# Kernel optimization log

Measured on AMD Instinct MI355X. Metric: run time of the kernel, lower is better.

## Reference

```python
import jax, jax.numpy as jnp
import numpy as np

N_BATCHES = 32
N_LABELS = 100


def setup_inputs() -> dict:
    key = jax.random.key(0)
    ks = jax.random.split(key, 7)
    N, D, P = 16384, 2048, 256
    x = jax.random.normal(ks[0], (N, D), dtype=jnp.float32)
    label = jax.random.randint(ks[1], (N,), 0, N_LABELS, dtype=jnp.int64)
    label_batch = jnp.sort(jax.random.randint(ks[2], (N,), 0, N_BATCHES, dtype=jnp.int64))
    W1_w = jax.random.normal(ks[3], (P, D), dtype=jnp.float32) * 0.02
    W1_b = jax.random.normal(ks[4], (P,), dtype=jnp.float32) * 0.02
    W2_w = jax.random.normal(ks[5], (P, D), dtype=jnp.float32) * 0.02
    W2_b = jax.random.normal(ks[6], (P,), dtype=jnp.float32) * 0.02
    return {"x": x, "label": label, "label_batch": label_batch,
            "W1_w": W1_w, "W1_b": W1_b, "W2_w": W2_w, "W2_b": W2_b}


def _loo_diff_label_mean(x, label, label_batch):
    # For each sample i: mean of x over {j : label_batch[j]==label_batch[i] and label[j]!=label[i]}.
    # Rows with no such j are zero (torch code's `continue`). x is detached in the original.
    N = x.shape[0]
    xs = jax.lax.stop_gradient(x)
    seg = label_batch * N_LABELS + label                      # combined (group,label) key
    n_seg = N_BATCHES * N_LABELS
    ones = jnp.ones((N,), dtype=x.dtype)
    sum_bl = jax.ops.segment_sum(xs, seg, num_segments=n_seg)            # [n_seg, D]
    cnt_bl = jax.ops.segment_sum(ones, seg, num_segments=n_seg)          # [n_seg]
    sum_b = jax.ops.segment_sum(xs, label_batch, num_segments=N_BATCHES)  # [NB, D]
    cnt_b = jax.ops.segment_sum(ones, label_batch, num_segments=N_BATCHES)
    diff_sum = sum_b[label_batch] - sum_bl[seg]               # [N, D]
    diff_cnt = cnt_b[label_batch] - cnt_bl[seg]               # [N]
    safe = jnp.maximum(diff_cnt, 1.0)
    mean = diff_sum / safe[:, None]
    return jnp.where((diff_cnt > 0)[:, None], mean, jnp.zeros_like(mean))


def reference(x, label, label_batch, W1_w, W1_b, W2_w, W2_b):
    calc_mean = _loo_diff_label_mean(x, label, label_batch)   # detached aggregate
    return x @ W1_w.T + W1_b + calc_mean @ W2_w.T + W2_b      # W1(x) + W2(mean)
```

## Files before the change

### kernel.cpp

```cpp
#include <hip/hip_runtime.h>
#include <cstdint>

#define N_SAMPLES 16384
#define DIM 2048
#define PDIM 256
#define NB 32
#define NL 100
#define NSEG (NB * NL)

typedef float floatx4 __attribute__((ext_vector_type(4)));
typedef __bf16 bf16x8 __attribute__((ext_vector_type(8)));

__device__ __forceinline__ unsigned short f32_to_bf16(float f) {
    unsigned int u = __float_as_uint(f);
    u += 0x7fffu + ((u >> 16) & 1u);
    return (unsigned short)(u >> 16);
}
__device__ __forceinline__ unsigned int pack_bf16x2(float a, float b) {
    return (unsigned int)f32_to_bf16(a) | ((unsigned int)f32_to_bf16(b) << 16);
}

__global__ __launch_bounds__(256) void prep_kernel(
    const float* __restrict__ W1w, const float* __restrict__ W1b,
    const float* __restrict__ W2w, const float* __restrict__ W2b,
    const int* __restrict__ label, const int* __restrict__ lbatch,
    unsigned short* __restrict__ W1bf, unsigned short* __restrict__ W2bf,
    float* __restrict__ bias, int* __restrict__ seg,
    int* __restrict__ hist, float* __restrict__ MW2)
{
    int i = blockIdx.x * 256 + threadIdx.x;
    W1bf[i] = f32_to_bf16(W1w[i]);
    W2bf[i] = f32_to_bf16(W2w[i]);
    if (i < PDIM) bias[i] = W1b[i] + W2b[i];
    if (i < N_SAMPLES) seg[i] = lbatch[i] * NL + label[i];
    if (i < NSEG) hist[i] = 0;
    if (i < NSEG * PDIM / 2) ((float2*)MW2)[i] = make_float2(0.f, 0.f);
}

__global__ __launch_bounds__(256) void hist_kernel(
    const int* __restrict__ seg, int* __restrict__ hist)
{
    int i = blockIdx.x * 256 + threadIdx.x;
    atomicAdd(&hist[seg[i]], 1);
}

#define SCAN_BPT 13
__global__ __launch_bounds__(256) void scan_kernel(
    const int* __restrict__ hist, int* __restrict__ offs, int* __restrict__ cursor)
{
    __shared__ int ps[256];
    const int t = threadIdx.x;
    int local = 0;
    #pragma unroll
    for (int k = 0; k < SCAN_BPT; ++k) {
        int bin = t * SCAN_BPT + k;
        if (bin < NSEG) local += hist[bin];
    }
    ps[t] = local;
    __syncthreads();
    for (int d = 1; d < 256; d <<= 1) {
        int v = (t >= d) ? ps[t - d] : 0;
        __syncthreads();
        ps[t] += v;
        __syncthreads();
    }
    int run = ps[t] - local;
    #pragma unroll
    for (int k = 0; k < SCAN_BPT; ++k) {
        int bin = t * SCAN_BPT + k;
        if (bin < NSEG) {
            offs[bin] = run;
            cursor[bin] = run;
            run += hist[bin];
        }
    }
    if (t == 255) offs[NSEG] = ps[255];
}

__global__ __launch_bounds__(256) void scatter_kernel(
    const int* __restrict__ seg, int* __restrict__ cursor, int* __restrict__ perm)
{
    int i = blockIdx.x * 256 + threadIdx.x;
    int pos = atomicAdd(&cursor[seg[i]], 1);
    perm[pos] = i;
}

__global__ __launch_bounds__(256) void segsum_kernel(
    const float* __restrict__ x, const int* __restrict__ perm,
    const int* __restrict__ offs,
    unsigned short* __restrict__ xb, float* __restrict__ sum_bl)
{
    const int tid = threadIdx.x;
    const int w = tid >> 6, lane = tid & 63;
    const int s = blockIdx.y * 4 + w;
    const int c = blockIdx.x * 512 + lane * 8;
    const int beg = offs[s], end = offs[s + 1];

    floatx4 sum0 = {0.f, 0.f, 0.f, 0.f};
    floatx4 sum1 = {0.f, 0.f, 0.f, 0.f};
    for (int base = beg; base < end; base += 64) {
        int p = (base + lane < end) ? perm[base + lane] : 0;
        const int n = min(end - base, 64);
        for (int j0 = 0; j0 < n; j0 += 8) {
            int rr[8];
            floatx4 v0[8], v1[8];
            #pragma unroll
            for (int j = 0; j < 8; ++j) {
                rr[j] = __shfl(p, min(j0 + j, n - 1));
                const float* px = &x[(size_t)rr[j] * DIM + c];
                v0[j] = *(const floatx4*)px;
                v1[j] = *(const floatx4*)(px + 4);
            }
            #pragma unroll
            for (int j = 0; j < 8; ++j) {
                if (j < n - j0) {
                    sum0 += v0[j];
                    sum1 += v1[j];
                    uint4 o;
                    o.x = pack_bf16x2(v0[j][0], v0[j][1]);
                    o.y = pack_bf16x2(v0[j][2], v0[j][3]);
                    o.z = pack_bf16x2(v1[j][0], v1[j][1]);
                    o.w = pack_bf16x2(v1[j][2], v1[j][3]);
                    *(uint4*)&xb[(size_t)rr[j] * DIM + c] = o;
                }
            }
        }
    }
    *(floatx4*)&sum_bl[(size_t)s * DIM + c] = sum0;
    *(floatx4*)&sum_bl[(size_t)s * DIM + c + 4] = sum1;
}

__global__ __launch_bounds__(256) void meanm_kernel(
    const float* __restrict__ sum_bl, const int* __restrict__ offs,
    unsigned short* __restrict__ Mb)
{
    __shared__ float acc[NL][256];
    const int tid = threadIdx.x;
    const int b = blockIdx.y;
    const int c = blockIdx.x * 256 + tid;

    float tot = 0.f;
    for (int l0 = 0; l0 < NL; l0 += 4) {
        float v[4];
        #pragma unroll
        for (int j = 0; j < 4; ++j)
            v[j] = sum_bl[(size_t)(b * NL + l0 + j) * DIM + c];
        #pragma unroll
        for (int j = 0; j < 4; ++j) { acc[l0 + j][tid] = v[j]; tot += v[j]; }
    }

    const int ob = offs[b * NL];
    const int cb = offs[(b + 1) * NL] - ob;
    for (int l = 0; l < NL; ++l) {
        int dc = cb - (offs[b * NL + l + 1] - offs[b * NL + l]);
        float m = (dc > 0) ? (tot - acc[l][tid]) / (float)dc : 0.f;
        Mb[(size_t)(b * NL + l) * DIM + c] = f32_to_bf16(m);
    }
}

template<int BM, int BN, int WR, int WC, bool FUSE, int KSPLIT>
__global__ __launch_bounds__(256) void gemm_bt_kernel(
    const unsigned short* __restrict__ A,
    const unsigned short* __restrict__ B,
    float* __restrict__ C,
    const float* __restrict__ bias,
    const float* __restrict__ add,
    const int* __restrict__ seg,
    int K)
{
    constexpr int SM = BM / WR, SN = BN / WC;
    constexpr int FM = SM / 16, FN = SN / 16;
    __shared__ __align__(16) unsigned short ldsA[BM * 32];
    __shared__ __align__(16) unsigned short ldsB[BN * 32];
    const int tid = threadIdx.x;
    const int lane = tid & 63;
    const int wave = tid >> 6;
    const int wr = wave / WC, wc = wave % WC;
    const int quad = lane >> 4, l15 = lane & 15;
    const int m0 = blockIdx.x * BM;
    const int n0 = blockIdx.y * BN;
    const int kpw = K / KSPLIT;
    const int k0 = blockIdx.z * kpw;
    const int srow = lane >> 2, schunk = lane & 3;

    floatx4 acc[FM][FN];
    #pragma unroll
    for (int i = 0; i < FM; ++i)
        #pragma unroll
        for (int j = 0; j < FN; ++j) acc[i][j] = (floatx4){0.f, 0.f, 0.f, 0.f};

    const unsigned short* Abase = A + (size_t)(m0 + srow) * K + schunk * 8;
    const unsigned short* Bbase = B + (size_t)(n0 + srow) * K + schunk * 8;

    for (int kk = k0; kk < k0 + kpw; kk += 32) {
        __syncthreads();
        #pragma unroll
        for (int ch = wave; ch < BM / 16; ch += 4)
            __builtin_amdgcn_global_load_lds(
                (const __attribute__((address_space(1))) void*)(Abase + (size_t)ch * 16 * K + kk),
                (__attribute__((address_space(3))) void*)&ldsA[ch * 16 * 32], 16, 0, 0);
        #pragma unroll
        for (int ch = wave; ch < BN / 16; ch += 4)
            __builtin_amdgcn_global_load_lds(
                (const __attribute__((address_space(1))) void*)(Bbase + (size_t)ch * 16 * K + kk),
                (__attribute__((address_space(3))) void*)&ldsB[ch * 16 * 32], 16, 0, 0);
        __syncthreads();

        bf16x8 af[FM], bfr[FN];
        #pragma unroll
        for (int mi = 0; mi < FM; ++mi)
            af[mi] = *(const bf16x8*)&ldsA[(wr * SM + mi * 16 + l15) * 32 + quad * 8];
        #pragma unroll
        for (int ni = 0; ni < FN; ++ni)
            bfr[ni] = *(const bf16x8*)&ldsB[(wc * SN + ni * 16 + l15) * 32 + quad * 8];
        #pragma unroll
        for (int mi = 0; mi < FM; ++mi)
            #pragma unroll
            for (int ni = 0; ni < FN; ++ni)
                acc[mi][ni] = __builtin_amdgcn_mfma_f32_16x16x32_bf16(
                    af[mi], bfr[ni], acc[mi][ni], 0, 0, 0);
    }

    #pragma unroll
    for (int mi = 0; mi < FM; ++mi) {
        const int rbase = m0 + wr * SM + mi * 16 + quad * 4;
        #pragma unroll
        for (int ni = 0; ni < FN; ++ni) {
            const int col = n0 + wc * SN + ni * 16 + l15;
            float bsum = 0.f;
            if constexpr (FUSE) bsum = bias[col];
            #pragma unroll
            for (int r = 0; r < 4; ++r) {
                const int row = rbase + r;
                float v = acc[mi][ni][r];
                if constexpr (FUSE) v += bsum + add[(size_t)seg[row] * PDIM + col];
                if constexpr (KSPLIT > 1)
                    atomicAdd(&C[(size_t)row * PDIM + col], v);
                else
                    C[(size_t)row * PDIM + col] = v;
            }
        }
    }
}

extern "C" void kernel_launch(void* const* d_in, const int* in_sizes, int n_in,
                              void* d_out, int out_size, void* d_ws, size_t ws_size,
                              hipStream_t stream)
{
    const float* x      = (const float*)d_in[0];
    const int*   label  = (const int*)d_in[1];
    const int*   lbatch = (const int*)d_in[2];
    const float* W1w    = (const float*)d_in[3];
    const float* W1b    = (const float*)d_in[4];
    const float* W2w    = (const float*)d_in[5];
    const float* W2b    = (const float*)d_in[6];
    float* out = (float*)d_out;

    char* ws = (char*)d_ws;
    size_t off = 0;
    auto alloc = [&](size_t bytes) {
        void* p = ws + off;
        off = (off + bytes + 255) & ~(size_t)255;
        return p;
    };
    unsigned short* xb   = (unsigned short*)alloc((size_t)N_SAMPLES * DIM * 2);
    unsigned short* Mb   = (unsigned short*)alloc((size_t)NSEG * DIM * 2);
    unsigned short* W1bf = (unsigned short*)alloc((size_t)PDIM * DIM * 2);
    unsigned short* W2bf = (unsigned short*)alloc((size_t)PDIM * DIM * 2);
    float* MW2    = (float*)alloc((size_t)NSEG * PDIM * 4);
    float* sum_bl = (float*)alloc((size_t)NSEG * DIM * 4);
    float* bias   = (float*)alloc(PDIM * 4);
    int*   seg    = (int*)alloc(N_SAMPLES * 4);
    int*   perm   = (int*)alloc(N_SAMPLES * 4);
    int*   hist   = (int*)alloc(NSEG * 4);
    int*   offs   = (int*)alloc((NSEG + 1) * 4);
    int*   cursor = (int*)alloc(NSEG * 4);

    prep_kernel<<<PDIM * DIM / 256, 256, 0, stream>>>(
        W1w, W1b, W2w, W2b, label, lbatch, W1bf, W2bf, bias, seg, hist, MW2);

    hist_kernel<<<N_SAMPLES / 256, 256, 0, stream>>>(seg, hist);
    scan_kernel<<<1, 256, 0, stream>>>(hist, offs, cursor);
    scatter_kernel<<<N_SAMPLES / 256, 256, 0, stream>>>(seg, cursor, perm);

    segsum_kernel<<<dim3(DIM / 512, NSEG / 4), 256, 0, stream>>>(
        x, perm, offs, xb, sum_bl);

    meanm_kernel<<<dim3(DIM / 256, NB), 256, 0, stream>>>(sum_bl, offs, Mb);

    gemm_bt_kernel<32, 256, 1, 4, false, 2>
        <<<dim3(NSEG / 32, 1, 2), 256, 0, stream>>>(
        Mb, W2bf, MW2, nullptr, nullptr, nullptr, DIM);

    gemm_bt_kernel<64, 128, 2, 2, true, 1>
        <<<dim3(N_SAMPLES / 64, PDIM / 128), 256, 0, stream>>>(
        xb, W1bf, out, bias, MW2, seg, DIM);
}
```

Measured before the change: 316.6 us.

## Project segment sums through W2 before leave-one-out mean to shrink finalize work

Moves the leave-one-out mean computation after the W2 projection: segment sums are stored as bf16 and multiplied by W2 directly, then a small finalize kernel computes (total - own)/count in the 256-wide projected space. This drops the fp32 sum_bl buffer and the 2048-wide meanm pass, which read and wrote large NSEG x DIM arrays. The trade-off is that sums are rounded to bf16 instead of means, which can lose precision for large segment sums, and the finalize kernel runs on only 32 blocks.

```diff
diff --git a/kernel.cpp b/kernel.cpp
--- a/kernel.cpp
+++ b/kernel.cpp
@@ -26,7 +26,7 @@
     const int* __restrict__ label, const int* __restrict__ lbatch,
     unsigned short* __restrict__ W1bf, unsigned short* __restrict__ W2bf,
     float* __restrict__ bias, int* __restrict__ seg,
-    int* __restrict__ hist, float* __restrict__ MW2)
+    int* __restrict__ hist, float* __restrict__ SW2)
 {
     int i = blockIdx.x * 256 + threadIdx.x;
     W1bf[i] = f32_to_bf16(W1w[i]);
@@ -34,7 +34,7 @@
     if (i < PDIM) bias[i] = W1b[i] + W2b[i];
     if (i < N_SAMPLES) seg[i] = lbatch[i] * NL + label[i];
     if (i < NSEG) hist[i] = 0;
-    if (i < NSEG * PDIM / 2) ((float2*)MW2)[i] = make_float2(0.f, 0.f);
+    if (i < NSEG * PDIM / 2) ((float2*)SW2)[i] = make_float2(0.f, 0.f);
 }
 
 __global__ __launch_bounds__(256) void hist_kernel(
@@ -88,7 +88,7 @@
 __global__ __launch_bounds__(256) void segsum_kernel(
     const float* __restrict__ x, const int* __restrict__ perm,
     const int* __restrict__ offs,
-    unsigned short* __restrict__ xb, float* __restrict__ sum_bl)
+    unsigned short* __restrict__ xb, unsigned short* __restrict__ sumb)
 {
     const int tid = threadIdx.x;
     const int w = tid >> 6, lane = tid & 63;
@@ -126,35 +126,29 @@
             }
         }
     }
-    *(floatx4*)&sum_bl[(size_t)s * DIM + c] = sum0;
-    *(floatx4*)&sum_bl[(size_t)s * DIM + c + 4] = sum1;
-}
-
-__global__ __launch_bounds__(256) void meanm_kernel(
-    const float* __restrict__ sum_bl, const int* __restrict__ offs,
-    unsigned short* __restrict__ Mb)
-{
-    __shared__ float acc[NL][256];
-    const int tid = threadIdx.x;
-    const int b = blockIdx.y;
-    const int c = blockIdx.x * 256 + tid;
-
+    uint4 so;
+    so.x = pack_bf16x2(sum0[0], sum0[1]);
+    so.y = pack_bf16x2(sum0[2], sum0[3]);
+    so.z = pack_bf16x2(sum1[0], sum1[1]);
+    so.w = pack_bf16x2(sum1[2], sum1[3]);
+    *(uint4*)&sumb[(size_t)s * DIM + c] = so;
+}
+
+__global__ __launch_bounds__(256) void finalize_kernel(
+    float* __restrict__ SW2, const int* __restrict__ offs)
+{
+    const int b = blockIdx.x;
+    const int col = threadIdx.x;
+    const int cb = offs[(b + 1) * NL] - offs[b * NL];
     float tot = 0.f;
-    for (int l0 = 0; l0 < NL; l0 += 4) {
-        float v[4];
-        #pragma unroll
-        for (int j = 0; j < 4; ++j)
-            v[j] = sum_bl[(size_t)(b * NL + l0 + j) * DIM + c];
-        #pragma unroll
-        for (int j = 0; j < 4; ++j) { acc[l0 + j][tid] = v[j]; tot += v[j]; }
-    }
-
-    const int ob = offs[b * NL];
-    const int cb = offs[(b + 1) * NL] - ob;
+    #pragma unroll 4
+    for (int l = 0; l < NL; ++l)
+        tot += SW2[(size_t)(b * NL + l) * PDIM + col];
     for (int l = 0; l < NL; ++l) {
-        int dc = cb - (offs[b * NL + l + 1] - offs[b * NL + l]);
-        float m = (dc > 0) ? (tot - acc[l][tid]) / (float)dc : 0.f;
-        Mb[(size_t)(b * NL + l) * DIM + c] = f32_to_bf16(m);
+        const int s = b * NL + l;
+        const int dc = cb - (offs[s + 1] - offs[s]);
+        const float v = SW2[(size_t)s * PDIM + col];
+        SW2[(size_t)s * PDIM + col] = (dc > 0) ? (tot - v) / (float)dc : 0.f;
     }
 }
 
@@ -264,11 +258,10 @@
         return p;
     };
     unsigned short* xb   = (unsigned short*)alloc((size_t)N_SAMPLES * DIM * 2);
-    unsigned short* Mb   = (unsigned short*)alloc((size_t)NSEG * DIM * 2);
+    unsigned short* sumb = (unsigned short*)alloc((size_t)NSEG * DIM * 2);
     unsigned short* W1bf = (unsigned short*)alloc((size_t)PDIM * DIM * 2);
     unsigned short* W2bf = (unsigned short*)alloc((size_t)PDIM * DIM * 2);
-    float* MW2    = (float*)alloc((size_t)NSEG * PDIM * 4);
-    float* sum_bl = (float*)alloc((size_t)NSEG * DIM * 4);
+    float* SW2    = (float*)alloc((size_t)NSEG * PDIM * 4);
     float* bias   = (float*)alloc(PDIM * 4);
     int*   seg    = (int*)alloc(N_SAMPLES * 4);
     int*   perm   = (int*)alloc(N_SAMPLES * 4);
@@ -277,22 +270,22 @@
     int*   cursor = (int*)alloc(NSEG * 4);
 
     prep_kernel<<<PDIM * DIM / 256, 256, 0, stream>>>(
-        W1w, W1b, W2w, W2b, label, lbatch, W1bf, W2bf, bias, seg, hist, MW2);
+        W1w, W1b, W2w, W2b, label, lbatch, W1bf, W2bf, bias, seg, hist, SW2);
 
     hist_kernel<<<N_SAMPLES / 256, 256, 0, stream>>>(seg, hist);
     scan_kernel<<<1, 256, 0, stream>>>(hist, offs, cursor);
     scatter_kernel<<<N_SAMPLES / 256, 256, 0, stream>>>(seg, cursor, perm);
 
     segsum_kernel<<<dim3(DIM / 512, NSEG / 4), 256, 0, stream>>>(
-        x, perm, offs, xb, sum_bl);
-
-    meanm_kernel<<<dim3(DIM / 256, NB), 256, 0, stream>>>(sum_bl, offs, Mb);
+        x, perm, offs, xb, sumb);
 
     gemm_bt_kernel<32, 256, 1, 4, false, 2>
         <<<dim3(NSEG / 32, 1, 2), 256, 0, stream>>>(
-        Mb, W2bf, MW2, nullptr, nullptr, nullptr, DIM);
+        sumb, W2bf, SW2, nullptr, nullptr, nullptr, DIM);
+
+    finalize_kernel<<<NB, 256, 0, stream>>>(SW2, offs);
 
     gemm_bt_kernel<64, 128, 2, 2, true, 1>
         <<<dim3(N_SAMPLES / 64, PDIM / 128), 256, 0, stream>>>(
-        xb, W1bf, out, bias, MW2, seg, DIM);
-}
+        xb, W1bf, out, bias, SW2, seg, DIM);
+}
```

Result: no change. 316.3 us (-0.1%).
